# Performance work log

Hardware: AMD Instinct MI355X
Metric: run time of the kernel (lower is better)

The kernel has to match this reference:

```python
import jax, jax.numpy as jnp
import numpy as np

EMBED = 1024
HEADS = 16
HEAD_DIM = EMBED // HEADS


def setup_inputs() -> dict:
    key = jax.random.key(0)
    ks = jax.random.split(key, 11)
    B, S = 4, 2048
    scale = 1.0 / np.sqrt(EMBED)
    inp = {
        "query": jax.random.normal(ks[0], (B, S, EMBED), dtype=jnp.float32),
        "key": jax.random.normal(ks[1], (B, S, EMBED), dtype=jnp.float32),
        "value": jax.random.normal(ks[2], (B, S, EMBED), dtype=jnp.float32),
        "Wq": jax.random.normal(ks[3], (EMBED, EMBED), dtype=jnp.float32) * scale,
        "bq": jnp.zeros((EMBED,), dtype=jnp.float32),
        "Wk": jax.random.normal(ks[4], (EMBED, EMBED), dtype=jnp.float32) * scale,
        "bk": jnp.zeros((EMBED,), dtype=jnp.float32),
        "Wv": jax.random.normal(ks[5], (EMBED, EMBED), dtype=jnp.float32) * scale,
        "bv": jnp.zeros((EMBED,), dtype=jnp.float32),
        "Wo": jax.random.normal(ks[6], (EMBED, EMBED), dtype=jnp.float32) * scale,
        "bo": jnp.zeros((EMBED,), dtype=jnp.float32),
    }
    return inp


def _split_heads(x):
    # [B,S,E] -> [B,H,S,D]
    B, S, _ = x.shape
    return x.reshape(B, S, HEADS, HEAD_DIM).transpose(0, 2, 1, 3)


def reference(query, key, value, Wq, bq, Wk, bk, Wv, bv, Wo, bo):
    B, S, _ = query.shape
    q = _split_heads(query @ Wq.T + bq)   # [B,H,S,D]
    k = _split_heads(key @ Wk.T + bk)
    v = _split_heads(value @ Wv.T + bv)
    scores = jnp.einsum("bhqd,bhkd->bhqk", q, k) / jnp.sqrt(jnp.float32(HEAD_DIM))
    attn = jax.nn.softmax(scores, axis=-1)
    out = jnp.einsum("bhqk,bhkd->bhqd", attn, v)  # [B,H,S,D]
    out = out.transpose(0, 2, 1, 3).reshape(B, S, EMBED)
    return out @ Wo.T + bo
```

## Files before the change

kernel.cpp:

```cpp
#include <hip/hip_runtime.h>

typedef _Float16 f16;
typedef __attribute__((ext_vector_type(2))) __fp16 fp16x2_raw;
typedef __attribute__((ext_vector_type(4))) _Float16 f16x4;
typedef __attribute__((ext_vector_type(8))) _Float16 f16x8;
typedef __attribute__((ext_vector_type(4))) float f32x4;
typedef __attribute__((ext_vector_type(16))) float f32x16;
typedef __attribute__((ext_vector_type(2))) unsigned int u32x2;
typedef __attribute__((ext_vector_type(4))) unsigned int u32x4;

#define NB 4
#define NS 2048
#define NE 1024
#define NH 16
#define ND 64
#define NM (NB*NS)

__device__ __forceinline__ void gld16(const void* g, void* l) {
  __builtin_amdgcn_global_load_lds((const __attribute__((address_space(1))) unsigned int*)g,
                                   (__attribute__((address_space(3))) unsigned int*)l, 16, 0, 0);
}

__device__ __forceinline__ unsigned cvt2h(float a, float b) {
  fp16x2_raw r = __builtin_amdgcn_cvt_pkrtz(a, b);
  return __builtin_bit_cast(unsigned, r);
}

__device__ __forceinline__ void plswap(unsigned& a, unsigned& b) {
  asm volatile("v_permlane32_swap_b32 %0, %1" : "+v"(a), "+v"(b));
}

__device__ __forceinline__ u32x4 pack8(float4 x0, float4 x1) {
  u32x4 r;
  r[0] = cvt2h(x0.x, x0.y); r[1] = cvt2h(x0.z, x0.w);
  r[2] = cvt2h(x1.x, x1.y); r[3] = cvt2h(x1.z, x1.w);
  return r;
}

template<bool AF32, bool OUTF32>
__device__ __forceinline__
void gemm_body(const void* __restrict__ Asrc, const float* __restrict__ Bsrc,
               const float* __restrict__ bias, float* __restrict__ Cf,
               f16* __restrict__ Ch, int id, f16* As, f16* Bs)
{
  const int K = NE, N = NE;
  const int t = threadIdx.x;
  const int l = t & 63, w = t >> 6;
  const int wr = w >> 1, wc = w & 1;

  const int xcd = id & 7, slot = id >> 3;
  const int m0 = (((slot >> 3) << 3) | xcd) * 128;
  const int n0 = (slot & 7) * 128;

  f32x4 acc[4][4];
  #pragma unroll
  for (int i = 0; i < 4; ++i)
    #pragma unroll
    for (int j = 0; j < 4; ++j)
      acc[i][j] = f32x4{0.f, 0.f, 0.f, 0.f};

  const int off0 = (w*2+0)*1024 + l*16;
  const int off1 = (w*2+1)*1024 + l*16;
  const int row0 = off0 >> 6, k0 = (off0 & 63) >> 1;
  const int row1 = off1 >> 6, k1 = (off1 & 63) >> 1;
  const f16*   a0h = (const f16*)Asrc   + (size_t)(m0+row0)*K + k0;
  const f16*   a1h = (const f16*)Asrc   + (size_t)(m0+row1)*K + k1;
  const float* a0f = (const float*)Asrc + (size_t)(m0+row0)*K + k0;
  const float* a1f = (const float*)Asrc + (size_t)(m0+row1)*K + k1;
  const float* b0f = Bsrc + (size_t)(n0+row0)*K + k0;
  const float* b1f = Bsrc + (size_t)(n0+row1)*K + k1;

  const int aoff = (wr*64 + (l&15))*32 + ((l>>4)<<3);
  const int boff = (wc*64 + (l&15))*32 + ((l>>4)<<3);

  float4 B0x0, B0x1, B0y0, B0y1, B1x0, B1x1, B1y0, B1y1;
  float4 A0x0, A0x1, A0y0, A0y1, A1x0, A1x1, A1y0, A1y1;
  f16x8  H0a, H0b, H1a, H1b;

  {
    B0x0 = *(const float4*)(b0f);     B0x1 = *(const float4*)(b0f + 4);
    B0y0 = *(const float4*)(b1f);     B0y1 = *(const float4*)(b1f + 4);
    *(u32x4*)(Bs + off0/2) = pack8(B0x0, B0x1);
    *(u32x4*)(Bs + off1/2) = pack8(B0y0, B0y1);
    if constexpr (AF32) {
      A0x0 = *(const float4*)(a0f);   A0x1 = *(const float4*)(a0f + 4);
      A0y0 = *(const float4*)(a1f);   A0y1 = *(const float4*)(a1f + 4);
      *(u32x4*)(As + off0/2) = pack8(A0x0, A0x1);
      *(u32x4*)(As + off1/2) = pack8(A0y0, A0y1);
    } else {
      H0a = *(const f16x8*)(a0h);     H0b = *(const f16x8*)(a1h);
      *(f16x8*)(As + off0/2) = H0a;
      *(f16x8*)(As + off1/2) = H0b;
    }
    B1x0 = *(const float4*)(b0f + 32);  B1x1 = *(const float4*)(b0f + 36);
    B1y0 = *(const float4*)(b1f + 32);  B1y1 = *(const float4*)(b1f + 36);
    if constexpr (AF32) {
      A1x0 = *(const float4*)(a0f + 32);  A1x1 = *(const float4*)(a0f + 36);
      A1y0 = *(const float4*)(a1f + 32);  A1y1 = *(const float4*)(a1f + 36);
    } else {
      H1a = *(const f16x8*)(a0h + 32);    H1b = *(const f16x8*)(a1h + 32);
    }
  }
  __syncthreads();

  #define GB_COMPUTE(BUFOFF)                                                     \
    {                                                                            \
      const f16* Ac = As + (BUFOFF);                                             \
      const f16* Bc = Bs + (BUFOFF);                                             \
      f16x8 af[4], bf[4];                                                        \
      _Pragma("unroll")                                                          \
      for (int i = 0; i < 4; ++i) af[i] = *(const f16x8*)(Ac + aoff + i*512);    \
      _Pragma("unroll")                                                          \
      for (int j = 0; j < 4; ++j) bf[j] = *(const f16x8*)(Bc + boff + j*512);    \
      _Pragma("unroll")                                                          \
      for (int i = 0; i < 4; ++i)                                                \
        _Pragma("unroll")                                                        \
        for (int j = 0; j < 4; ++j)                                              \
          acc[i][j] = __builtin_amdgcn_mfma_f32_16x16x32_f16(af[i], bf[j], acc[i][j], 0, 0, 0); \
    }

  for (int ksi = 0; ksi < 32; ksi += 2) {
    const bool ld0 = (ksi + 2 < 32);
    if (ld0) {
      const int kt = (ksi + 2) * 32;
      B0x0 = *(const float4*)(b0f + kt);  B0x1 = *(const float4*)(b0f + kt + 4);
      B0y0 = *(const float4*)(b1f + kt);  B0y1 = *(const float4*)(b1f + kt + 4);
      if constexpr (AF32) {
        A0x0 = *(const float4*)(a0f + kt);  A0x1 = *(const float4*)(a0f + kt + 4);
        A0y0 = *(const float4*)(a1f + kt);  A0y1 = *(const float4*)(a1f + kt + 4);
      } else {
        H0a = *(const f16x8*)(a0h + kt);    H0b = *(const f16x8*)(a1h + kt);
      }
    }
    GB_COMPUTE(0)
    *(u32x4*)(Bs + 4096 + off0/2) = pack8(B1x0, B1x1);
    *(u32x4*)(Bs + 4096 + off1/2) = pack8(B1y0, B1y1);
    if constexpr (AF32) {
      *(u32x4*)(As + 4096 + off0/2) = pack8(A1x0, A1x1);
      *(u32x4*)(As + 4096 + off1/2) = pack8(A1y0, A1y1);
    } else {
      *(f16x8*)(As + 4096 + off0/2) = H1a;
      *(f16x8*)(As + 4096 + off1/2) = H1b;
    }
    __syncthreads();

    const bool ld1 = (ksi + 3 < 32);
    if (ld1) {
      const int kt = (ksi + 3) * 32;
      B1x0 = *(const float4*)(b0f + kt);  B1x1 = *(const float4*)(b0f + kt + 4);
      B1y0 = *(const float4*)(b1f + kt);  B1y1 = *(const float4*)(b1f + kt + 4);
      if constexpr (AF32) {
        A1x0 = *(const float4*)(a0f + kt);  A1x1 = *(const float4*)(a0f + kt + 4);
        A1y0 = *(const float4*)(a1f + kt);  A1y1 = *(const float4*)(a1f + kt + 4);
      } else {
        H1a = *(const f16x8*)(a0h + kt);    H1b = *(const f16x8*)(a1h + kt);
      }
    }
    GB_COMPUTE(4096)
    if (ld0) {
      *(u32x4*)(Bs + off0/2) = pack8(B0x0, B0x1);
      *(u32x4*)(Bs + off1/2) = pack8(B0y0, B0y1);
      if constexpr (AF32) {
        *(u32x4*)(As + off0/2) = pack8(A0x0, A0x1);
        *(u32x4*)(As + off1/2) = pack8(A0y0, A0y1);
      } else {
        *(f16x8*)(As + off0/2) = H0a;
        *(f16x8*)(As + off1/2) = H0b;
      }
    }
    __syncthreads();
  }
  #undef GB_COMPUTE

  #pragma unroll
  for (int j = 0; j < 4; ++j) {
    const int col = n0 + wc*64 + j*16 + (l & 15);
    const float bb = bias[col];
    #pragma unroll
    for (int i = 0; i < 4; ++i) {
      const int rowb = m0 + wr*64 + i*16 + ((l>>4)<<2);
      #pragma unroll
      for (int r = 0; r < 4; ++r) {
        float v = acc[i][j][r] + bb;
        if constexpr (OUTF32) Cf[(size_t)(rowb+r)*N + col] = v;
        else                  Ch[(size_t)(rowb+r)*N + col] = (f16)v;
      }
    }
  }
}

__global__ __launch_bounds__(256)
void gemm_qkv(const float* __restrict__ q_in, const float* __restrict__ k_in,
              const float* __restrict__ v_in, const float* __restrict__ Wq,
              const float* __restrict__ Wk, const float* __restrict__ Wv,
              const float* __restrict__ bq, const float* __restrict__ bk,
              const float* __restrict__ bv, f16* __restrict__ Qp,
              f16* __restrict__ Kp, f16* __restrict__ Vp)
{
  __shared__ __align__(16) f16 As[2*128*32];
  __shared__ __align__(16) f16 Bs[2*128*32];
  const int z = blockIdx.z;
  const float* Asrc = (z == 0) ? q_in : (z == 1) ? k_in : v_in;
  const float* Bsrc = (z == 0) ? Wq : (z == 1) ? Wk : Wv;
  const float* bias = (z == 0) ? bq : (z == 1) ? bk : bv;
  f16* Ch = (z == 0) ? Qp : (z == 1) ? Kp : Vp;
  const int id = blockIdx.x + blockIdx.y * gridDim.x;
  gemm_body<true, false>(Asrc, Bsrc, bias, nullptr, Ch, id, As, Bs);
}

__global__ __launch_bounds__(256)
void gemm_out(const f16* __restrict__ Op, const float* __restrict__ Wo,
              const float* __restrict__ bo, float* __restrict__ Out)
{
  __shared__ __align__(16) f16 As[2*128*32];
  __shared__ __align__(16) f16 Bs[2*128*32];
  const int id = blockIdx.x + blockIdx.y * gridDim.x;
  gemm_body<false, true>(Op, Wo, bo, Out, nullptr, id, As, Bs);
}

__global__ __launch_bounds__(256, 4)
void attn_kernel(const f16* __restrict__ Q, const f16* __restrict__ K,
                 const f16* __restrict__ V, f16* __restrict__ O)
{
  __shared__ __align__(16) f16 S_lds[16384];

  const int t = threadIdx.x, l = t & 63, w = t >> 6;
  const int lq = l & 31, hi = l >> 5;

  const int lin = blockIdx.x + (blockIdx.y << 4);
  const int xcd = lin & 7, jj = lin >> 3;
  const int bh = xcd * 8 + (jj >> 4);
  const int qt = jj & 15;
  const int b = bh >> 4, h = bh & 15;
  const size_t base = (size_t)b * NS * NE + (size_t)h * ND;
  const int q = qt*128 + w*32 + lq;

  f16x8 bq[4];
  #pragma unroll
  for (int ks = 0; ks < 4; ++ks)
    bq[ks] = *(const f16x8*)&Q[base + (size_t)q*NE + ks*16 + hi*8];
  asm volatile("s_waitcnt vmcnt(0)" ::: "memory");

  f32x16 o[2];
  #pragma unroll
  for (int dt = 0; dt < 2; ++dt)
    #pragma unroll
    for (int r = 0; r < 16; ++r) o[dt][r] = 0.f;
  float m2 = -3e38f, lsum = 0.f;
  const float K2 = 0.125f * 1.44269504089f;

  const int krow0 = w*16 + (l>>3);
  const int kgran = ((l&7) ^ (l>>3)) * 8;
  const f16* kSrc0 = K + base + (size_t)krow0*NE + kgran;
  const f16* kSrc1 = kSrc0 + (size_t)8*NE;
  const f16* vSrc = V + base + (size_t)l*NE + w*16;

  const size_t tileAdv = (size_t)64 * NE;
  const int kd0 = (w*2+0)*512 + l*8;
  const int kd1 = (w*2+1)*512 + l*8;

  f16x8 va, vb;
  {
    gld16(kSrc0, &S_lds[0] + kd0);
    gld16(kSrc1, &S_lds[0] + kd1);
    va = *(const f16x8*)(vSrc);
    vb = *(const f16x8*)(vSrc + 8);
    asm volatile("s_waitcnt vmcnt(0)" ::: "memory");
    char* vt0 = (char*)&S_lds[4096];
    #pragma unroll
    for (int i = 0; i < 8; ++i) {
      const int d0 = w*16 + i, d1 = w*16 + 8 + i;
      *(f16*)(vt0 + ((d0*128 + l*2) ^ ((i & 7) << 4))) = va[i];
      *(f16*)(vt0 + ((d1*128 + l*2) ^ ((i & 7) << 4))) = vb[i];
    }
  }
  __syncthreads();

  for (int it = 0; it < 32; ++it) {
    const int cur = it & 1, nb = cur ^ 1;
    const char* ksb = (const char*)(&S_lds[cur*8192]);
    const char* vtb = (const char*)(&S_lds[cur*8192 + 4096]);

    if (it < 31) {
      const size_t g = (size_t)(it+1) * tileAdv;
      gld16(kSrc0 + g, &S_lds[nb*8192] + kd0);
      gld16(kSrc1 + g, &S_lds[nb*8192] + kd1);
      va = *(const f16x8*)(vSrc + g);
      vb = *(const f16x8*)(vSrc + g + 8);
    }

    f32x16 s[2];
    #pragma unroll
    for (int ct = 0; ct < 2; ++ct)
      #pragma unroll
      for (int r = 0; r < 16; ++r) s[ct][r] = 0.f;
    __builtin_amdgcn_s_setprio(1);
    #pragma unroll
    for (int ct = 0; ct < 2; ++ct) {
      const int krow = ct*32 + lq;
      const int rswz = (krow & 7) << 4;
      #pragma unroll
      for (int ks = 0; ks < 4; ++ks) {
        f16x8 ak = *(const f16x8*)(ksb + ((krow*128 + ks*32 + hi*16) ^ rswz));
        s[ct] = __builtin_amdgcn_mfma_f32_32x32x16_f16(ak, bq[ks], s[ct], 0, 0, 0);
      }
    }
    __builtin_amdgcn_s_setprio(0);

    float mm[16];
    #pragma unroll
    for (int r = 0; r < 16; ++r) mm[r] = fmaxf(s[0][r], s[1][r]);
    #pragma unroll
    for (int st = 8; st > 0; st >>= 1)
      #pragma unroll
      for (int r = 0; r < st; ++r) mm[r] = fmaxf(mm[r], mm[r+st]);
    float mx = mm[0] * K2;
    mx = fmaxf(mx, __shfl_xor(mx, 32));

    if (__any(mx > m2 + 8.0f)) {
      const float mnew = fmaxf(m2, mx);
      const float alpha = __builtin_amdgcn_exp2f(m2 - mnew);
      m2 = mnew;
      lsum *= alpha;
      #pragma unroll
      for (int dt = 0; dt < 2; ++dt)
        #pragma unroll
        for (int r = 0; r < 16; ++r) o[dt][r] *= alpha;
    }

    float ps4[4] = {0.f, 0.f, 0.f, 0.f};
    #pragma unroll
    for (int ct = 0; ct < 2; ++ct)
      #pragma unroll
      for (int r = 0; r < 16; ++r) {
        float p = __builtin_amdgcn_exp2f(s[ct][r]*K2 - m2);
        s[ct][r] = p;
        ps4[r & 3] += p;
      }
    lsum += (ps4[0] + ps4[1]) + (ps4[2] + ps4[3]);

    f16x8 pa[4];
    #pragma unroll
    for (int ct = 0; ct < 2; ++ct) {
      unsigned wd[8];
      #pragma unroll
      for (int m = 0; m < 4; ++m)
        #pragma unroll
        for (int hh = 0; hh < 2; ++hh)
          wd[m*2 + hh] = cvt2h(s[ct][4*m + 2*hh], s[ct][4*m + 2*hh + 1]);
      #pragma unroll
      for (int ks2 = 0; ks2 < 2; ++ks2) {
        unsigned a0 = wd[(2*ks2)*2 + 0], b0 = wd[(2*ks2+1)*2 + 0];
        unsigned a1 = wd[(2*ks2)*2 + 1], b1 = wd[(2*ks2+1)*2 + 1];
        plswap(a0, b0);
        plswap(a1, b1);
        union { unsigned u[4]; f16x8 v; } pp;
        pp.u[0] = a0; pp.u[1] = a1; pp.u[2] = b0; pp.u[3] = b1;
        pa[ct*2 + ks2] = pp.v;
      }
    }

    __builtin_amdgcn_s_setprio(1);
    #pragma unroll
    for (int ks = 0; ks < 4; ++ks)
      #pragma unroll
      for (int dt = 0; dt < 2; ++dt) {
        const int drow = dt*32 + lq;
        f16x8 av = *(const f16x8*)(vtb + ((drow*128 + ks*32 + hi*16) ^ ((drow & 7) << 4)));
        o[dt] = __builtin_amdgcn_mfma_f32_32x32x16_f16(av, pa[ks], o[dt], 0, 0, 0);
      }
    __builtin_amdgcn_s_setprio(0);

    if (it < 31) {
      asm volatile("s_waitcnt vmcnt(0)" ::: "memory");
      char* vtn = (char*)(&S_lds[nb*8192 + 4096]);
      #pragma unroll
      for (int i = 0; i < 8; ++i) {
        const int d0 = w*16 + i, d1 = w*16 + 8 + i;
        *(f16*)(vtn + ((d0*128 + l*2) ^ ((i & 7) << 4))) = va[i];
        *(f16*)(vtn + ((d1*128 + l*2) ^ ((i & 7) << 4))) = vb[i];
      }
      __syncthreads();
    }
  }

  const float lt = lsum + __shfl_xor(lsum, 32);
  const float linv = 1.0f / lt;
  #pragma unroll
  for (int dt = 0; dt < 2; ++dt)
    #pragma unroll
    for (int m = 0; m < 4; ++m) {
      u32x2 st;
      st.x = cvt2h(o[dt][4*m+0]*linv, o[dt][4*m+1]*linv);
      st.y = cvt2h(o[dt][4*m+2]*linv, o[dt][4*m+3]*linv);
      const int d = dt*32 + 8*m + 4*hi;
      *(u32x2*)&O[base + (size_t)q*NE + d] = st;
    }
}

extern "C" void kernel_launch(void* const* d_in, const int* in_sizes, int n_in,
                              void* d_out, int out_size, void* d_ws, size_t ws_size,
                              hipStream_t stream)
{
  const float* q_in = (const float*)d_in[0];
  const float* k_in = (const float*)d_in[1];
  const float* v_in = (const float*)d_in[2];
  const float* Wq = (const float*)d_in[3];
  const float* bq = (const float*)d_in[4];
  const float* Wk = (const float*)d_in[5];
  const float* bk = (const float*)d_in[6];
  const float* Wv = (const float*)d_in[7];
  const float* bv = (const float*)d_in[8];
  const float* Wo = (const float*)d_in[9];
  const float* bo = (const float*)d_in[10];

  char* ws = (char*)d_ws;
  f16* Qp   = (f16*)(ws + 58720256);
  f16* Kp   = (f16*)(ws + 75497472);
  f16* Vp   = (f16*)(ws + 92274688);
  f16* Op   = (f16*)(ws + 109051904);

  gemm_qkv<<<dim3(8, 64, 3), 256, 0, stream>>>(q_in, k_in, v_in, Wq, Wk, Wv,
                                               bq, bk, bv, Qp, Kp, Vp);

  attn_kernel<<<dim3(16, 64), 256, 0, stream>>>(Qp, Kp, Vp, Op);

  gemm_out<<<dim3(8, 64), 256, 0, stream>>>(Op, Wo, bo, (float*)d_out);
}
```

Measured before the change: 219.1 us.

## Pre-convert weights to fp16 once and stream B tiles via global_load_lds

Adds a kernel that converts all four fp32 weight matrices to fp16 in workspace before the GEMMs. The GEMMs then load B tiles with direct global-to-LDS 16-byte loads instead of loading fp32 into registers, packing, and storing to LDS. This halves weight bytes per tile and frees registers and VALU work, at the cost of an extra launch and a full weight conversion pass each call. The async LDS writes rely on the existing barriers for ordering, with no explicit waits added.

```diff
diff --git a/kernel.cpp b/kernel.cpp
--- a/kernel.cpp
+++ b/kernel.cpp
@@ -37,9 +37,29 @@
   return r;
 }
 
+__global__ __launch_bounds__(256) void cvt_w(const float* __restrict__ s3, const float* __restrict__ s4,
+                                             const float* __restrict__ s5, const float* __restrict__ s6,
+                                             f16* __restrict__ dst) {
+  const int W = NE*NE/4;
+  const int total = 4*W;
+  int idx = blockIdx.x * blockDim.x + threadIdx.x;
+  int stride = gridDim.x * blockDim.x;
+  for (int i = idx; i < total; i += stride) {
+    const float* src; int off;
+    if      (i <   W)   { src = s3; off = i; }
+    else if (i < 2*W)   { src = s4; off = i - W; }
+    else if (i < 3*W)   { src = s5; off = i - 2*W; }
+    else                { src = s6; off = i - 3*W; }
+    float4 v = ((const float4*)src)[off];
+    f16x4 o;
+    o[0] = (_Float16)v.x; o[1] = (_Float16)v.y; o[2] = (_Float16)v.z; o[3] = (_Float16)v.w;
+    ((f16x4*)dst)[i] = o;
+  }
+}
+
 template<bool AF32, bool OUTF32>
 __device__ __forceinline__
-void gemm_body(const void* __restrict__ Asrc, const float* __restrict__ Bsrc,
+void gemm_body(const void* __restrict__ Asrc, const f16* __restrict__ Bw,
                const float* __restrict__ bias, float* __restrict__ Cf,
                f16* __restrict__ Ch, int id, f16* As, f16* Bs)
 {
@@ -67,39 +87,29 @@
   const f16*   a1h = (const f16*)Asrc   + (size_t)(m0+row1)*K + k1;
   const float* a0f = (const float*)Asrc + (size_t)(m0+row0)*K + k0;
   const float* a1f = (const float*)Asrc + (size_t)(m0+row1)*K + k1;
-  const float* b0f = Bsrc + (size_t)(n0+row0)*K + k0;
-  const float* b1f = Bsrc + (size_t)(n0+row1)*K + k1;
+  const f16* b0 = Bw + (size_t)(n0+row0)*K + k0;
+  const f16* b1 = Bw + (size_t)(n0+row1)*K + k1;
 
   const int aoff = (wr*64 + (l&15))*32 + ((l>>4)<<3);
   const int boff = (wc*64 + (l&15))*32 + ((l>>4)<<3);
 
-  float4 B0x0, B0x1, B0y0, B0y1, B1x0, B1x1, B1y0, B1y1;
   float4 A0x0, A0x1, A0y0, A0y1, A1x0, A1x1, A1y0, A1y1;
   f16x8  H0a, H0b, H1a, H1b;
 
-  {
-    B0x0 = *(const float4*)(b0f);     B0x1 = *(const float4*)(b0f + 4);
-    B0y0 = *(const float4*)(b1f);     B0y1 = *(const float4*)(b1f + 4);
-    *(u32x4*)(Bs + off0/2) = pack8(B0x0, B0x1);
-    *(u32x4*)(Bs + off1/2) = pack8(B0y0, B0y1);
-    if constexpr (AF32) {
-      A0x0 = *(const float4*)(a0f);   A0x1 = *(const float4*)(a0f + 4);
-      A0y0 = *(const float4*)(a1f);   A0y1 = *(const float4*)(a1f + 4);
-      *(u32x4*)(As + off0/2) = pack8(A0x0, A0x1);
-      *(u32x4*)(As + off1/2) = pack8(A0y0, A0y1);
-    } else {
-      H0a = *(const f16x8*)(a0h);     H0b = *(const f16x8*)(a1h);
-      *(f16x8*)(As + off0/2) = H0a;
-      *(f16x8*)(As + off1/2) = H0b;
-    }
-    B1x0 = *(const float4*)(b0f + 32);  B1x1 = *(const float4*)(b0f + 36);
-    B1y0 = *(const float4*)(b1f + 32);  B1y1 = *(const float4*)(b1f + 36);
-    if constexpr (AF32) {
-      A1x0 = *(const float4*)(a0f + 32);  A1x1 = *(const float4*)(a0f + 36);
-      A1y0 = *(const float4*)(a1f + 32);  A1y1 = *(const float4*)(a1f + 36);
-    } else {
-      H1a = *(const f16x8*)(a0h + 32);    H1b = *(const f16x8*)(a1h + 32);
-    }
+  gld16(b0, Bs + off0/2);
+  gld16(b1, Bs + off1/2);
+  if constexpr (AF32) {
+    A0x0 = *(const float4*)(a0f);   A0x1 = *(const float4*)(a0f + 4);
+    A0y0 = *(const float4*)(a1f);   A0y1 = *(const float4*)(a1f + 4);
+    *(u32x4*)(As + off0/2) = pack8(A0x0, A0x1);
+    *(u32x4*)(As + off1/2) = pack8(A0y0, A0y1);
+    A1x0 = *(const float4*)(a0f + 32);  A1x1 = *(const float4*)(a0f + 36);
+    A1y0 = *(const float4*)(a1f + 32);  A1y1 = *(const float4*)(a1f + 36);
+  } else {
+    H0a = *(const f16x8*)(a0h);     H0b = *(const f16x8*)(a1h);
+    *(f16x8*)(As + off0/2) = H0a;
+    *(f16x8*)(As + off1/2) = H0b;
+    H1a = *(const f16x8*)(a0h + 32);    H1b = *(const f16x8*)(a1h + 32);
   }
   __syncthreads();
 
@@ -121,10 +131,13 @@
 
   for (int ksi = 0; ksi < 32; ksi += 2) {
     const bool ld0 = (ksi + 2 < 32);
+    {
+      const int kt1 = (ksi + 1) * 32;
+      gld16(b0 + kt1, Bs + 4096 + off0/2);
+      gld16(b1 + kt1, Bs + 4096 + off1/2);
+    }
     if (ld0) {
       const int kt = (ksi + 2) * 32;
-      B0x0 = *(const float4*)(b0f + kt);  B0x1 = *(const float4*)(b0f + kt + 4);
-      B0y0 = *(const float4*)(b1f + kt);  B0y1 = *(const float4*)(b1f + kt + 4);
       if constexpr (AF32) {
         A0x0 = *(const float4*)(a0f + kt);  A0x1 = *(const float4*)(a0f + kt + 4);
         A0y0 = *(const float4*)(a1f + kt);  A0y1 = *(const float4*)(a1f + kt + 4);
@@ -133,8 +146,6 @@
       }
     }
     GB_COMPUTE(0)
-    *(u32x4*)(Bs + 4096 + off0/2) = pack8(B1x0, B1x1);
-    *(u32x4*)(Bs + 4096 + off1/2) = pack8(B1y0, B1y1);
     if constexpr (AF32) {
       *(u32x4*)(As + 4096 + off0/2) = pack8(A1x0, A1x1);
       *(u32x4*)(As + 4096 + off1/2) = pack8(A1y0, A1y1);
@@ -145,10 +156,13 @@
     __syncthreads();
 
     const bool ld1 = (ksi + 3 < 32);
+    if (ld0) {
+      const int kt2 = (ksi + 2) * 32;
+      gld16(b0 + kt2, Bs + off0/2);
+      gld16(b1 + kt2, Bs + off1/2);
+    }
     if (ld1) {
       const int kt = (ksi + 3) * 32;
-      B1x0 = *(const float4*)(b0f + kt);  B1x1 = *(const float4*)(b0f + kt + 4);
-      B1y0 = *(const float4*)(b1f + kt);  B1y1 = *(const float4*)(b1f + kt + 4);
       if constexpr (AF32) {
         A1x0 = *(const float4*)(a0f + kt);  A1x1 = *(const float4*)(a0f + kt + 4);
         A1y0 = *(const float4*)(a1f + kt);  A1y1 = *(const float4*)(a1f + kt + 4);
@@ -158,8 +172,6 @@
     }
     GB_COMPUTE(4096)
     if (ld0) {
-      *(u32x4*)(Bs + off0/2) = pack8(B0x0, B0x1);
-      *(u32x4*)(Bs + off1/2) = pack8(B0y0, B0y1);
       if constexpr (AF32) {
         *(u32x4*)(As + off0/2) = pack8(A0x0, A0x1);
         *(u32x4*)(As + off1/2) = pack8(A0y0, A0y1);
@@ -191,8 +203,7 @@
 
 __global__ __launch_bounds__(256)
 void gemm_qkv(const float* __restrict__ q_in, const float* __restrict__ k_in,
-              const float* __restrict__ v_in, const float* __restrict__ Wq,
-              const float* __restrict__ Wk, const float* __restrict__ Wv,
+              const float* __restrict__ v_in, const f16* __restrict__ W16,
               const float* __restrict__ bq, const float* __restrict__ bk,
               const float* __restrict__ bv, f16* __restrict__ Qp,
               f16* __restrict__ Kp, f16* __restrict__ Vp)
@@ -201,21 +212,21 @@
   __shared__ __align__(16) f16 Bs[2*128*32];
   const int z = blockIdx.z;
   const float* Asrc = (z == 0) ? q_in : (z == 1) ? k_in : v_in;
-  const float* Bsrc = (z == 0) ? Wq : (z == 1) ? Wk : Wv;
+  const f16* Bw = W16 + (size_t)z * NE * NE;
   const float* bias = (z == 0) ? bq : (z == 1) ? bk : bv;
   f16* Ch = (z == 0) ? Qp : (z == 1) ? Kp : Vp;
   const int id = blockIdx.x + blockIdx.y * gridDim.x;
-  gemm_body<true, false>(Asrc, Bsrc, bias, nullptr, Ch, id, As, Bs);
+  gemm_body<true, false>(Asrc, Bw, bias, nullptr, Ch, id, As, Bs);
 }
 
 __global__ __launch_bounds__(256)
-void gemm_out(const f16* __restrict__ Op, const float* __restrict__ Wo,
+void gemm_out(const f16* __restrict__ Op, const f16* __restrict__ Wo16,
               const float* __restrict__ bo, float* __restrict__ Out)
 {
   __shared__ __align__(16) f16 As[2*128*32];
   __shared__ __align__(16) f16 Bs[2*128*32];
   const int id = blockIdx.x + blockIdx.y * gridDim.x;
-  gemm_body<false, true>(Op, Wo, bo, Out, nullptr, id, As, Bs);
+  gemm_body<false, true>(Op, Wo16, bo, Out, nullptr, id, As, Bs);
 }
 
 __global__ __launch_bounds__(256, 4)
@@ -415,15 +426,18 @@
   const float* bo = (const float*)d_in[10];
 
   char* ws = (char*)d_ws;
+  f16* W16  = (f16*)(ws + 50331648);
   f16* Qp   = (f16*)(ws + 58720256);
   f16* Kp   = (f16*)(ws + 75497472);
   f16* Vp   = (f16*)(ws + 92274688);
   f16* Op   = (f16*)(ws + 109051904);
 
-  gemm_qkv<<<dim3(8, 64, 3), 256, 0, stream>>>(q_in, k_in, v_in, Wq, Wk, Wv,
+  cvt_w<<<1024, 256, 0, stream>>>(Wq, Wk, Wv, Wo, W16);
+
+  gemm_qkv<<<dim3(8, 64, 3), 256, 0, stream>>>(q_in, k_in, v_in, W16,
                                                bq, bk, bv, Qp, Kp, Vp);
 
   attn_kernel<<<dim3(16, 64), 256, 0, stream>>>(Qp, Kp, Vp, Op);
 
-  gemm_out<<<dim3(8, 64), 256, 0, stream>>>(Op, Wo, bo, (float*)d_out);
-}
+  gemm_out<<<dim3(8, 64), 256, 0, stream>>>(Op, W16 + (size_t)3*NE*NE, bo, (float*)d_out);
+}
```

New measurement: 225.1 us. +2.8%, slower.
